# Optimization experiments

Measured on AMD Instinct MI355X. Metric: run time of the kernel, lower is better.

## Reference

```python
import jax, jax.numpy as jnp
import numpy as np

# Dims: batch B, seq L, embed D, router hidden H, num_blocks NB, top_k K
B, L, D, H, NB, K = 8, 4096, 1024, 64, 16, 2
TEMP = 2.0          # current_temperature buffer (init 2.0), clamp(min=0.1) inert
LN_EPS = 1e-5


def setup_inputs() -> dict:
    key = jax.random.key(0)
    k_x, k_w1, k_w2 = jax.random.split(key, 3)
    return {
        "x": jax.random.normal(k_x, (B, L, D), dtype=jnp.float32),
        "ln_gamma": jnp.ones((D,), dtype=jnp.float32),
        "ln_beta": jnp.zeros((D,), dtype=jnp.float32),
        "W1": jax.random.normal(k_w1, (D, H), dtype=jnp.float32) / np.sqrt(D).astype(np.float32),
        "W2": jax.random.normal(k_w2, (H, NB), dtype=jnp.float32) / np.sqrt(H).astype(np.float32),
    }


def reference(x, ln_gamma, ln_beta, W1, W2):
    # gate: LayerNorm -> Linear(no bias) -> GELU(exact) -> Linear(no bias)
    mu = jnp.mean(x, axis=-1, keepdims=True)
    var = jnp.mean(jnp.square(x - mu), axis=-1, keepdims=True)
    xn = (x - mu) * jax.lax.rsqrt(var + LN_EPS) * ln_gamma + ln_beta
    h = jax.nn.gelu(xn @ W1, approximate=False)          # (B, L, H)
    logits = (h @ W2) / TEMP                              # (B, L, NB)

    probs = jax.nn.softmax(logits, axis=-1)               # (B, L, NB)
    top_probs, indices = jax.lax.top_k(probs, K)          # (B, L, K) each
    weights = top_probs / (jnp.sum(top_probs, axis=-1, keepdims=True) + 1e-8)

    # load-balancing aux loss: f = fraction of assignments per block (detached),
    # P = mean router prob per block
    counts = jnp.zeros((NB,), dtype=probs.dtype).at[indices.reshape(-1)].add(1.0)
    f = jax.lax.stop_gradient(counts) / (B * L * K + 1e-8)
    P = jnp.mean(probs, axis=(0, 1))                      # (NB,)
    aux_loss = NB * jnp.sum(f * P)

    return probs, indices, aux_loss, weights
```

## Files before the change

### kernel.cpp

```cpp
#include <hip/hip_runtime.h>
#include <math.h>

typedef __attribute__((ext_vector_type(8))) short short8;
typedef __attribute__((ext_vector_type(4))) float f32x4;

#define NTOK 32768
#define DDIM 1024
#define HDIM 64
#define NB 16
#define LN_EPS 1e-5f

#define IDX_OFF ((size_t)NTOK * NB)
#define AUX_OFF (IDX_OFF + (size_t)NTOK * 2)
#define WT_OFF  (AUX_OFF + 1)

#define CS_F   64
#define BP_F   4352
#define PART_F 102656

__device__ __forceinline__ short8 as_s8(uint4 u) {
    union { uint4 u; short8 s; } x; x.u = u; return x.s;
}

__device__ __forceinline__ f32x4 ntload4(const float* p) {
    return __builtin_nontemporal_load((const f32x4*)p);
}

__device__ __forceinline__ void gld16(const void* g, float* l) {
    __builtin_amdgcn_global_load_lds(
        (const __attribute__((address_space(1))) void*)g,
        (__attribute__((address_space(3))) void*)l, 16, 0, 0);
}

__global__ void pack_kernel(const float* __restrict__ W1,
                            const float* __restrict__ gamma,
                            const float* __restrict__ beta,
                            float* __restrict__ ws) {
    __shared__ float sg[4][64];
    __shared__ float sb[4][64];
    const int s = blockIdx.x;
    const int t = threadIdx.x;

    {
        const int j = t & 63, p = t >> 6;
        float ag = 0.f, ab = 0.f;
        for (int kk = 0; kk < 8; ++kk) {
            const int k = s * 32 + p * 8 + kk;
            const float w = W1[k * HDIM + j];
            ag += gamma[k] * w;
            ab += beta[k] * w;
        }
        sg[p][j] = ag;
        sb[p][j] = ab;
    }

    {
        unsigned int* bp = (unsigned int*)(ws + BP_F);
        const int n = t >> 6;
        const int l = t & 63;
        const int q = l >> 4, c = l & 15;
        const int col = n * 16 + c;
        unsigned int uh[8], um[8], ul[8];
#pragma unroll
        for (int j = 0; j < 8; ++j) {
            const int k = s * 32 + q * 8 + j;
            const float w = gamma[k] * W1[k * HDIM + col];
            const unsigned int hb = __float_as_uint(w) & 0xFFFF0000u;
            const float r = w - __uint_as_float(hb);
            const unsigned int mb = __float_as_uint(r) & 0xFFFF0000u;
            const float r2 = r - __uint_as_float(mb);
            const unsigned int lb = __float_as_uint(r2) & 0xFFFF0000u;
            uh[j] = hb >> 16; um[j] = mb >> 16; ul[j] = lb >> 16;
        }
        const int base = ((s * 4 + n) * 64 + l) * 4;
#pragma unroll
        for (int d = 0; d < 4; ++d) {
            bp[base + d]         = uh[2 * d] | (uh[2 * d + 1] << 16);
            bp[32768 + base + d] = um[2 * d] | (um[2 * d + 1] << 16);
            bp[65536 + base + d] = ul[2 * d] | (ul[2 * d + 1] << 16);
        }
    }
    __syncthreads();
    if (t < 64) {
        atomicAdd(&ws[CS_F + t],      sg[0][t] + sg[1][t] + sg[2][t] + sg[3][t]);
        atomicAdd(&ws[CS_F + 64 + t], sb[0][t] + sb[1][t] + sb[2][t] + sb[3][t]);
    }
}

__device__ __forceinline__ void split8(const f32x4 a0, const f32x4 a1,
                                       short8& AH, short8& AM, short8& AL,
                                       float& s1, float& s2) {
    const float v[8] = {a0.x, a0.y, a0.z, a0.w, a1.x, a1.y, a1.z, a1.w};
    unsigned int ph[4], pm[4], pl[4];
#pragma unroll
    for (int d = 0; d < 4; ++d) {
        const float v0 = v[2 * d], v1 = v[2 * d + 1];
        const unsigned int h0 = __float_as_uint(v0) & 0xFFFF0000u;
        const unsigned int h1 = __float_as_uint(v1) & 0xFFFF0000u;
        const float r0 = v0 - __uint_as_float(h0);
        const float r1 = v1 - __uint_as_float(h1);
        const unsigned int m0 = __float_as_uint(r0) & 0xFFFF0000u;
        const unsigned int m1 = __float_as_uint(r1) & 0xFFFF0000u;
        const float q0 = r0 - __uint_as_float(m0);
        const float q1 = r1 - __uint_as_float(m1);
        ph[d] = (h0 >> 16) | h1;
        pm[d] = (m0 >> 16) | m1;
        pl[d] = (__float_as_uint(q0) >> 16) | (__float_as_uint(q1) & 0xFFFF0000u);
        s1 += v0 + v1;
        s2 = fmaf(v0, v0, fmaf(v1, v1, s2));
    }
    AH = as_s8(make_uint4(ph[0], ph[1], ph[2], ph[3]));
    AM = as_s8(make_uint4(pm[0], pm[1], pm[2], pm[3]));
    AL = as_s8(make_uint4(pl[0], pl[1], pl[2], pl[3]));
}

#define MFMA6(ACC, AH, AM, AL, BH, BM, BL)                                        \
    ACC = __builtin_amdgcn_mfma_f32_16x16x32_bf16(AH, as_s8(BH), ACC, 0, 0, 0);   \
    ACC = __builtin_amdgcn_mfma_f32_16x16x32_bf16(AH, as_s8(BM), ACC, 0, 0, 0);   \
    ACC = __builtin_amdgcn_mfma_f32_16x16x32_bf16(AM, as_s8(BH), ACC, 0, 0, 0);   \
    ACC = __builtin_amdgcn_mfma_f32_16x16x32_bf16(AH, as_s8(BL), ACC, 0, 0, 0);   \
    ACC = __builtin_amdgcn_mfma_f32_16x16x32_bf16(AM, as_s8(BM), ACC, 0, 0, 0);   \
    ACC = __builtin_amdgcn_mfma_f32_16x16x32_bf16(AL, as_s8(BH), ACC, 0, 0, 0);

#define PUB()                                                       \
    asm volatile("s_waitcnt vmcnt(0) lgkmcnt(0)" ::: "memory");     \
    __builtin_amdgcn_s_barrier();                                   \
    __builtin_amdgcn_sched_barrier(0)

#define A_F 0
#define A_BSTRIDE 8704
#define B_F 17408
#define B_BSTRIDE 6144
__global__ __launch_bounds__(512, 2)
void router_main(const float* __restrict__ x,
                 const float* __restrict__ ws_ro,
                 const unsigned int* __restrict__ bp,
                 const float* __restrict__ W2,
                 float* __restrict__ part,
                 float* __restrict__ out) {
    __shared__ __align__(16) float smem[29696];
    float* hlds = smem;
    float* w2l  = smem + 8320;
    float* llds = smem + 9344;
    float* cntl = smem + 11904;

    const int t    = threadIdx.x;
    const int wv   = t >> 6;
    const int lane = t & 63;
    const int q = lane >> 4, c = lane & 15;
    const int tok0 = blockIdx.x * 128;
    const int tokw = tok0 + wv * 16;

    float csg[4], csb[4];
#pragma unroll
    for (int n = 0; n < 4; ++n) {
        csg[n] = ws_ro[CS_F + n * 16 + c];
        csb[n] = ws_ro[CS_F + 64 + n * 16 + c];
    }

    const int bidx0 = wv * 3;
    const float* xA = x + (size_t)(tokw + q) * DDIM + c * 4;
    float* awb       = smem + A_F + wv * 1088 + q * 68 + c * 4;
    const float* arb = smem + A_F + wv * 1088 + c * 68 + q * 8;

#define STAGE_B(CI)                                                              \
    {                                                                            \
        float* dst = smem + B_F + ((CI) & 1) * B_BSTRIDE;                        \
        _Pragma("unroll")                                                        \
        for (int i = 0; i < 3; ++i) {                                            \
            const int idx = bidx0 + i;                                           \
            const int st = (idx >= 12) ? 1 : 0;                                  \
            const int rem = idx - st * 12;                                       \
            const int term = rem >> 2, n = rem & 3;                              \
            gld16(bp + term * 32768 + (2 * (CI) + st) * 1024 + n * 256 + lane*4, \
                  dst + st * 3072 + term * 1024 + n * 256);                      \
        }                                                                        \
    }
#define STAGE_A(CI)                                                              \
    {                                                                            \
        const float* srcA = xA + (CI) * 64;                                      \
        ar0 = ntload4(srcA);                                                     \
        ar1 = ntload4(srcA + 4096);                                              \
        ar2 = ntload4(srcA + 8192);                                              \
        ar3 = ntload4(srcA + 12288);                                             \
    }
#define DS_WRITE_A(CI)                                                           \
    {                                                                            \
        float* dw = awb + ((CI) & 1) * A_BSTRIDE;                                \
        *(f32x4*)(dw)       = ar0;                                               \
        *(f32x4*)(dw + 272) = ar1;                                               \
        *(f32x4*)(dw + 544) = ar2;                                               \
        *(f32x4*)(dw + 816) = ar3;                                               \
    }
#define COMPUTE(CI)                                                              \
    {                                                                            \
        const float* Ab = arb + ((CI) & 1) * A_BSTRIDE;                          \
        const float* Bb = smem + B_F + ((CI) & 1) * B_BSTRIDE;                   \
        _Pragma("unroll")                                                        \
        for (int st = 0; st < 2; ++st) {                                         \
            const f32x4 a00 = *(const f32x4*)(Ab + st * 32);                     \
            const f32x4 a01 = *(const f32x4*)(Ab + st * 32 + 4);                 \
            short8 AH0, AM0, AL0;                                                \
            split8(a00, a01, AH0, AM0, AL0, s1a, s2a);                           \
            const float* Bs = Bb + st * 3072;                                    \
            _Pragma("unroll")                                                    \
            for (int n = 0; n < 4; ++n) {                                        \
                const uint4 bh = *(const uint4*)(Bs + n * 256 + lane * 4);       \
                const uint4 bm = *(const uint4*)(Bs + 1024 + n * 256 + lane*4);  \
                const uint4 bl = *(const uint4*)(Bs + 2048 + n * 256 + lane*4);  \
                MFMA6(acc[n], AH0, AM0, AL0, bh, bm, bl);                        \
            }                                                                    \
        }                                                                        \
    }

    f32x4 acc[4] = {{0.f,0.f,0.f,0.f},{0.f,0.f,0.f,0.f},{0.f,0.f,0.f,0.f},{0.f,0.f,0.f,0.f}};
    float s1a = 0.f, s2a = 0.f;
    f32x4 ar0, ar1, ar2, ar3;

    STAGE_A(0)
    STAGE_B(0)
    DS_WRITE_A(0)
    PUB();

#pragma unroll 1
    for (int ci = 0; ci < 16; ++ci) {
        if (ci < 15) {
            STAGE_A(ci + 1)
            STAGE_B(ci + 1)
            __builtin_amdgcn_sched_barrier(0);
        }
        COMPUTE(ci)
        if (ci < 15) {
            DS_WRITE_A(ci + 1)
            PUB();
        }
    }
    __syncthreads();

    s1a += __shfl_xor(s1a, 16, 64); s1a += __shfl_xor(s1a, 32, 64);
    s2a += __shfl_xor(s2a, 16, 64); s2a += __shfl_xor(s2a, 32, 64);

    if (t < 16) cntl[t] = 0.f;
    if (t < 256) *(float4*)(w2l + t * 4) = *(const float4*)(W2 + t * 4);

    {
        float* hw = hlds + wv * 1040;
#pragma unroll
        for (int r = 0; r < 4; ++r) {
            const int tt = q * 4 + r;
            const float S1A = __shfl(s1a, tt, 64), S2A = __shfl(s2a, tt, 64);
            const float muA = S1A * (1.0f / 1024.0f);
            const float rsA = 1.0f / sqrtf(S2A * (1.0f / 1024.0f) - muA * muA + LN_EPS);
#pragma unroll
            for (int n = 0; n < 4; ++n) {
                const float preA = rsA * (acc[n][r] - muA * csg[n]) + csb[n];
                hw[tt * 65 + n * 16 + c] =
                    0.5f * preA * (1.0f + erff(preA * 0.70710678118654752f));
            }
        }
    }
    __syncthreads();

    {
        const int m2 = t >> 2, o = (t & 3) * 4;
        const float* hrow = hlds + (m2 >> 4) * 1040 + (m2 & 15) * 65;
        f32x4 L0 = {0.f, 0.f, 0.f, 0.f};
#pragma unroll 8
        for (int j = 0; j < 64; ++j) {
            L0 += *(const f32x4*)(w2l + j * 16 + o) * hrow[j];
        }
        *(f32x4*)(llds + m2 * 20 + o) = L0 * 0.5f;
    }
    __syncthreads();

    if (t < 128) {
        float p[16];
        float mx = -1e30f;
#pragma unroll
        for (int i = 0; i < NB; ++i) { p[i] = llds[t * 20 + i]; mx = fmaxf(mx, p[i]); }
        float ssum = 0.f;
#pragma unroll
        for (int i = 0; i < NB; ++i) { p[i] = expf(p[i] - mx); ssum += p[i]; }
        const float inv = 1.0f / ssum;
#pragma unroll
        for (int i = 0; i < NB; ++i) { p[i] *= inv; llds[t * 20 + i] = p[i]; }

        float* po = out + (size_t)(tok0 + t) * NB;
#pragma unroll
        for (int u = 0; u < 4; ++u) {
            float4 v; v.x = p[u*4]; v.y = p[u*4+1]; v.z = p[u*4+2]; v.w = p[u*4+3];
            *(float4*)(po + u * 4) = v;
        }

        float b0 = -1.f, b1 = -1.f;
        int i0 = 0, i1 = 0;
#pragma unroll
        for (int i = 0; i < NB; ++i) {
            if (p[i] > b0)      { b1 = b0; i1 = i0; b0 = p[i]; i0 = i; }
            else if (p[i] > b1) { b1 = p[i]; i1 = i; }
        }
        const float wsum = b0 + b1 + 1e-8f;
        out[IDX_OFF + (size_t)(tok0 + t) * 2]     = (float)i0;
        out[IDX_OFF + (size_t)(tok0 + t) * 2 + 1] = (float)i1;
        out[WT_OFF + (size_t)(tok0 + t) * 2]      = b0 / wsum;
        out[WT_OFF + (size_t)(tok0 + t) * 2 + 1]  = b1 / wsum;
        atomicAdd(&cntl[i0], 1.0f);
        atomicAdd(&cntl[i1], 1.0f);
    }
    __syncthreads();

    if (t < 16) {
        float ps = 0.f;
        for (int m = 0; m < 128; ++m) ps += llds[m * 20 + t];
        part[(size_t)blockIdx.x * 32 + t]      = cntl[t];
        part[(size_t)blockIdx.x * 32 + 16 + t] = ps;
    }
}

__global__ void aux_kernel(const float* __restrict__ part,
                           float* __restrict__ gacc,
                           float* __restrict__ out) {
    __shared__ float red[8][32];
    __shared__ float flag;
    const int t = threadIdx.x;
    const int b = blockIdx.x;
    const int i = t & 31, rr = t >> 5;
    const int r0 = b * 16 + rr;
    red[rr][i] = part[(size_t)r0 * 32 + i] + part[(size_t)(r0 + 8) * 32 + i];
    __syncthreads();
    if (t < 32) {
        float tot = 0.f;
#pragma unroll
        for (int p = 0; p < 8; ++p) tot += red[p][t];
        atomicAdd(&gacc[t], tot);
    }
    __syncthreads();
    if (t == 0) {
        __threadfence();
        const unsigned int old = atomicAdd((unsigned int*)(gacc + 32), 1u);
        flag = (old == 15u) ? 1.f : 0.f;
    }
    __syncthreads();
    if (flag != 0.f) {
        if (t < 32) red[0][t] = atomicAdd(&gacc[t], 0.0f);
        __syncthreads();
        if (t == 0) {
            float a = 0.f;
            for (int k = 0; k < NB; ++k) {
                const float f = red[0][k] / (65536.0f + 1e-8f);
                const float P = red[0][16 + k] * (1.0f / 32768.0f);
                a += f * P;
            }
            out[AUX_OFF] = 16.0f * a;
        }
    }
}

extern "C" void kernel_launch(void* const* d_in, const int* in_sizes, int n_in,
                              void* d_out, int out_size, void* d_ws, size_t ws_size,
                              hipStream_t stream) {
    const float* x     = (const float*)d_in[0];
    const float* gamma = (const float*)d_in[1];
    const float* beta  = (const float*)d_in[2];
    const float* W1    = (const float*)d_in[3];
    const float* W2    = (const float*)d_in[4];
    float* out = (float*)d_out;
    float* ws  = (float*)d_ws;

    (void)hipMemsetAsync(ws, 0, 192 * sizeof(float), stream);
    pack_kernel<<<32, 256, 0, stream>>>(W1, gamma, beta, ws);
    router_main<<<NTOK / 128, 512, 0, stream>>>(x, ws, (const unsigned int*)(ws + BP_F),
                                                W2, ws + PART_F, out);
    aux_kernel<<<16, 256, 0, stream>>>(ws + PART_F, ws, out);
}
```

Baseline: 222.6 us.

## Halve router block size, single-buffer A in LDS, recompute LN column sums per block

Router blocks shrink from 512 threads and 128 tokens to 256 threads and 64 tokens, with a smaller shared-memory footprint. The A tile is now single-buffered with padded stride 65, and x is read with plain loads instead of nontemporal ones. The gamma/beta column sums move out of pack_kernel: each block recomputes them from W1 into LDS, which adds redundant reads of W1. Per-block aux partials are atomically added straight into global accumulators, so the aux kernel becomes one small block; this trades a two-stage reduction for more atomic contention.

```diff
diff --git a/kernel.cpp b/kernel.cpp
--- a/kernel.cpp
+++ b/kernel.cpp
@@ -14,16 +14,10 @@
 #define AUX_OFF (IDX_OFF + (size_t)NTOK * 2)
 #define WT_OFF  (AUX_OFF + 1)
 
-#define CS_F   64
 #define BP_F   4352
-#define PART_F 102656
 
 __device__ __forceinline__ short8 as_s8(uint4 u) {
     union { uint4 u; short8 s; } x; x.u = u; return x.s;
-}
-
-__device__ __forceinline__ f32x4 ntload4(const float* p) {
-    return __builtin_nontemporal_load((const f32x4*)p);
 }
 
 __device__ __forceinline__ void gld16(const void* g, float* l) {
@@ -34,56 +28,32 @@
 
 __global__ void pack_kernel(const float* __restrict__ W1,
                             const float* __restrict__ gamma,
-                            const float* __restrict__ beta,
                             float* __restrict__ ws) {
-    __shared__ float sg[4][64];
-    __shared__ float sb[4][64];
     const int s = blockIdx.x;
     const int t = threadIdx.x;
-
-    {
-        const int j = t & 63, p = t >> 6;
-        float ag = 0.f, ab = 0.f;
-        for (int kk = 0; kk < 8; ++kk) {
-            const int k = s * 32 + p * 8 + kk;
-            const float w = W1[k * HDIM + j];
-            ag += gamma[k] * w;
-            ab += beta[k] * w;
-        }
-        sg[p][j] = ag;
-        sb[p][j] = ab;
-    }
-
-    {
-        unsigned int* bp = (unsigned int*)(ws + BP_F);
-        const int n = t >> 6;
-        const int l = t & 63;
-        const int q = l >> 4, c = l & 15;
-        const int col = n * 16 + c;
-        unsigned int uh[8], um[8], ul[8];
-#pragma unroll
-        for (int j = 0; j < 8; ++j) {
-            const int k = s * 32 + q * 8 + j;
-            const float w = gamma[k] * W1[k * HDIM + col];
-            const unsigned int hb = __float_as_uint(w) & 0xFFFF0000u;
-            const float r = w - __uint_as_float(hb);
-            const unsigned int mb = __float_as_uint(r) & 0xFFFF0000u;
-            const float r2 = r - __uint_as_float(mb);
-            const unsigned int lb = __float_as_uint(r2) & 0xFFFF0000u;
-            uh[j] = hb >> 16; um[j] = mb >> 16; ul[j] = lb >> 16;
-        }
-        const int base = ((s * 4 + n) * 64 + l) * 4;
-#pragma unroll
-        for (int d = 0; d < 4; ++d) {
-            bp[base + d]         = uh[2 * d] | (uh[2 * d + 1] << 16);
-            bp[32768 + base + d] = um[2 * d] | (um[2 * d + 1] << 16);
-            bp[65536 + base + d] = ul[2 * d] | (ul[2 * d + 1] << 16);
-        }
-    }
-    __syncthreads();
-    if (t < 64) {
-        atomicAdd(&ws[CS_F + t],      sg[0][t] + sg[1][t] + sg[2][t] + sg[3][t]);
-        atomicAdd(&ws[CS_F + 64 + t], sb[0][t] + sb[1][t] + sb[2][t] + sb[3][t]);
+    unsigned int* bp = (unsigned int*)(ws + BP_F);
+    const int n = t >> 6;
+    const int l = t & 63;
+    const int q = l >> 4, c = l & 15;
+    const int col = n * 16 + c;
+    unsigned int uh[8], um[8], ul[8];
+#pragma unroll
+    for (int j = 0; j < 8; ++j) {
+        const int k = s * 32 + q * 8 + j;
+        const float w = gamma[k] * W1[k * HDIM + col];
+        const unsigned int hb = __float_as_uint(w) & 0xFFFF0000u;
+        const float r = w - __uint_as_float(hb);
+        const unsigned int mb = __float_as_uint(r) & 0xFFFF0000u;
+        const float r2 = r - __uint_as_float(mb);
+        const unsigned int lb = __float_as_uint(r2) & 0xFFFF0000u;
+        uh[j] = hb >> 16; um[j] = mb >> 16; ul[j] = lb >> 16;
+    }
+    const int base = ((s * 4 + n) * 64 + l) * 4;
+#pragma unroll
+    for (int d = 0; d < 4; ++d) {
+        bp[base + d]         = uh[2 * d] | (uh[2 * d + 1] << 16);
+        bp[32768 + base + d] = um[2 * d] | (um[2 * d + 1] << 16);
+        bp[65536 + base + d] = ul[2 * d] | (ul[2 * d + 1] << 16);
     }
 }
 
@@ -127,47 +97,63 @@
     __builtin_amdgcn_s_barrier();                                   \
     __builtin_amdgcn_sched_barrier(0)
 
-#define A_F 0
-#define A_BSTRIDE 8704
-#define B_F 17408
-#define B_BSTRIDE 6144
-__global__ __launch_bounds__(512, 2)
+__global__ __launch_bounds__(256, 2)
 void router_main(const float* __restrict__ x,
-                 const float* __restrict__ ws_ro,
+                 const float* __restrict__ W1,
+                 const float* __restrict__ gamma,
+                 const float* __restrict__ beta,
                  const unsigned int* __restrict__ bp,
                  const float* __restrict__ W2,
-                 float* __restrict__ part,
+                 float* __restrict__ gacc,
                  float* __restrict__ out) {
-    __shared__ __align__(16) float smem[29696];
-    float* hlds = smem;
-    float* w2l  = smem + 8320;
-    float* llds = smem + 9344;
-    float* cntl = smem + 11904;
+    __shared__ __align__(16) float smem[16592];
+    float* csgl = smem + 16448;
+    float* csbl = smem + 16512;
+    float* cntl = smem + 16576;
+    float* w2l  = smem;
+    float* llds = smem + 1024;
+    float* hlds = smem + 12288;
 
     const int t    = threadIdx.x;
     const int wv   = t >> 6;
     const int lane = t & 63;
     const int q = lane >> 4, c = lane & 15;
-    const int tok0 = blockIdx.x * 128;
+    const int tok0 = blockIdx.x * 64;
     const int tokw = tok0 + wv * 16;
 
-    float csg[4], csb[4];
-#pragma unroll
-    for (int n = 0; n < 4; ++n) {
-        csg[n] = ws_ro[CS_F + n * 16 + c];
-        csb[n] = ws_ro[CS_F + 64 + n * 16 + c];
-    }
-
-    const int bidx0 = wv * 3;
+    {
+        const int j = t & 63, p = t >> 6;
+        float ag = 0.f, ab = 0.f;
+#pragma unroll 4
+        for (int k = p; k < DDIM; k += 4) {
+            const float w = W1[k * HDIM + j];
+            ag = fmaf(gamma[k], w, ag);
+            ab = fmaf(beta[k],  w, ab);
+        }
+        float* red = smem + 12288;
+        red[p * 64 + j] = ag;
+        red[256 + p * 64 + j] = ab;
+        __syncthreads();
+        if (t < 64)
+            csgl[t] = red[t] + red[64 + t] + red[128 + t] + red[192 + t];
+        else if (t < 128) {
+            const int j2 = t - 64;
+            csbl[j2] = red[256 + j2] + red[320 + j2] + red[384 + j2] + red[448 + j2];
+        }
+        if (t < 16) cntl[t] = 0.f;
+        __syncthreads();
+    }
+
+    const int bidx0 = wv * 6;
     const float* xA = x + (size_t)(tokw + q) * DDIM + c * 4;
-    float* awb       = smem + A_F + wv * 1088 + q * 68 + c * 4;
-    const float* arb = smem + A_F + wv * 1088 + c * 68 + q * 8;
+    float* awb       = smem + 12288 + wv * 1040 + q * 65 + c * 4;
+    const float* arb = smem + 12288 + wv * 1040 + c * 65 + q * 8;
 
 #define STAGE_B(CI)                                                              \
     {                                                                            \
-        float* dst = smem + B_F + ((CI) & 1) * B_BSTRIDE;                        \
+        float* dst = smem + ((CI) & 1) * 6144;                                   \
         _Pragma("unroll")                                                        \
-        for (int i = 0; i < 3; ++i) {                                            \
+        for (int i = 0; i < 6; ++i) {                                            \
             const int idx = bidx0 + i;                                           \
             const int st = (idx >= 12) ? 1 : 0;                                  \
             const int rem = idx - st * 12;                                       \
@@ -179,27 +165,25 @@
 #define STAGE_A(CI)                                                              \
     {                                                                            \
         const float* srcA = xA + (CI) * 64;                                      \
-        ar0 = ntload4(srcA);                                                     \
-        ar1 = ntload4(srcA + 4096);                                              \
-        ar2 = ntload4(srcA + 8192);                                              \
-        ar3 = ntload4(srcA + 12288);                                             \
-    }
-#define DS_WRITE_A(CI)                                                           \
+        ar0 = *(const f32x4*)(srcA);                                             \
+        ar1 = *(const f32x4*)(srcA + 4096);                                      \
+        ar2 = *(const f32x4*)(srcA + 8192);                                      \
+        ar3 = *(const f32x4*)(srcA + 12288);                                     \
+    }
+#define DS_WRITE_A()                                                             \
     {                                                                            \
-        float* dw = awb + ((CI) & 1) * A_BSTRIDE;                                \
-        *(f32x4*)(dw)       = ar0;                                               \
-        *(f32x4*)(dw + 272) = ar1;                                               \
-        *(f32x4*)(dw + 544) = ar2;                                               \
-        *(f32x4*)(dw + 816) = ar3;                                               \
+        *(f32x4*)(awb)       = ar0;                                              \
+        *(f32x4*)(awb + 260) = ar1;                                              \
+        *(f32x4*)(awb + 520) = ar2;                                              \
+        *(f32x4*)(awb + 780) = ar3;                                              \
     }
 #define COMPUTE(CI)                                                              \
     {                                                                            \
-        const float* Ab = arb + ((CI) & 1) * A_BSTRIDE;                          \
-        const float* Bb = smem + B_F + ((CI) & 1) * B_BSTRIDE;                   \
+        const float* Bb = smem + ((CI) & 1) * 6144;                              \
         _Pragma("unroll")                                                        \
         for (int st = 0; st < 2; ++st) {                                         \
-            const f32x4 a00 = *(const f32x4*)(Ab + st * 32);                     \
-            const f32x4 a01 = *(const f32x4*)(Ab + st * 32 + 4);                 \
+            const f32x4 a00 = *(const f32x4*)(arb + st * 32);                    \
+            const f32x4 a01 = *(const f32x4*)(arb + st * 32 + 4);                \
             short8 AH0, AM0, AL0;                                                \
             split8(a00, a01, AH0, AM0, AL0, s1a, s2a);                           \
             const float* Bs = Bb + st * 3072;                                    \
@@ -219,7 +203,7 @@
 
     STAGE_A(0)
     STAGE_B(0)
-    DS_WRITE_A(0)
+    DS_WRITE_A()
     PUB();
 
 #pragma unroll 1
@@ -230,8 +214,10 @@
             __builtin_amdgcn_sched_barrier(0);
         }
         COMPUTE(ci)
+        asm volatile("s_waitcnt lgkmcnt(0)" ::: "memory");
+        __builtin_amdgcn_sched_barrier(0);
         if (ci < 15) {
-            DS_WRITE_A(ci + 1)
+            DS_WRITE_A()
             PUB();
         }
     }
@@ -240,8 +226,7 @@
     s1a += __shfl_xor(s1a, 16, 64); s1a += __shfl_xor(s1a, 32, 64);
     s2a += __shfl_xor(s2a, 16, 64); s2a += __shfl_xor(s2a, 32, 64);
 
-    if (t < 16) cntl[t] = 0.f;
-    if (t < 256) *(float4*)(w2l + t * 4) = *(const float4*)(W2 + t * 4);
+    *(float4*)(w2l + t * 4) = *(const float4*)(W2 + t * 4);
 
     {
         float* hw = hlds + wv * 1040;
@@ -253,7 +238,8 @@
             const float rsA = 1.0f / sqrtf(S2A * (1.0f / 1024.0f) - muA * muA + LN_EPS);
 #pragma unroll
             for (int n = 0; n < 4; ++n) {
-                const float preA = rsA * (acc[n][r] - muA * csg[n]) + csb[n];
+                const float preA = rsA * (acc[n][r] - muA * csgl[n * 16 + c])
+                                 + csbl[n * 16 + c];
                 hw[tt * 65 + n * 16 + c] =
                     0.5f * preA * (1.0f + erff(preA * 0.70710678118654752f));
             }
@@ -273,7 +259,7 @@
     }
     __syncthreads();
 
-    if (t < 128) {
+    if (t < 64) {
         float p[16];
         float mx = -1e30f;
 #pragma unroll
@@ -311,48 +297,26 @@
 
     if (t < 16) {
         float ps = 0.f;
-        for (int m = 0; m < 128; ++m) ps += llds[m * 20 + t];
-        part[(size_t)blockIdx.x * 32 + t]      = cntl[t];
-        part[(size_t)blockIdx.x * 32 + 16 + t] = ps;
-    }
-}
-
-__global__ void aux_kernel(const float* __restrict__ part,
-                           float* __restrict__ gacc,
+        for (int m = 0; m < 64; ++m) ps += llds[m * 20 + t];
+        atomicAdd(&gacc[t], cntl[t]);
+        atomicAdd(&gacc[16 + t], ps);
+    }
+}
+
+__global__ void aux_kernel(float* __restrict__ gacc,
                            float* __restrict__ out) {
-    __shared__ float red[8][32];
-    __shared__ float flag;
+    __shared__ float red[32];
     const int t = threadIdx.x;
-    const int b = blockIdx.x;
-    const int i = t & 31, rr = t >> 5;
-    const int r0 = b * 16 + rr;
-    red[rr][i] = part[(size_t)r0 * 32 + i] + part[(size_t)(r0 + 8) * 32 + i];
-    __syncthreads();
-    if (t < 32) {
-        float tot = 0.f;
-#pragma unroll
-        for (int p = 0; p < 8; ++p) tot += red[p][t];
-        atomicAdd(&gacc[t], tot);
-    }
+    if (t < 32) red[t] = atomicAdd(&gacc[t], 0.0f);
     __syncthreads();
     if (t == 0) {
-        __threadfence();
-        const unsigned int old = atomicAdd((unsigned int*)(gacc + 32), 1u);
-        flag = (old == 15u) ? 1.f : 0.f;
-    }
-    __syncthreads();
-    if (flag != 0.f) {
-        if (t < 32) red[0][t] = atomicAdd(&gacc[t], 0.0f);
-        __syncthreads();
-        if (t == 0) {
-            float a = 0.f;
-            for (int k = 0; k < NB; ++k) {
-                const float f = red[0][k] / (65536.0f + 1e-8f);
-                const float P = red[0][16 + k] * (1.0f / 32768.0f);
-                a += f * P;
-            }
-            out[AUX_OFF] = 16.0f * a;
-        }
+        float a = 0.f;
+        for (int k = 0; k < NB; ++k) {
+            const float f = red[k] / (65536.0f + 1e-8f);
+            const float P = red[16 + k] * (1.0f / 32768.0f);
+            a += f * P;
+        }
+        out[AUX_OFF] = 16.0f * a;
     }
 }
 
@@ -368,8 +332,9 @@
     float* ws  = (float*)d_ws;
 
     (void)hipMemsetAsync(ws, 0, 192 * sizeof(float), stream);
-    pack_kernel<<<32, 256, 0, stream>>>(W1, gamma, beta, ws);
-    router_main<<<NTOK / 128, 512, 0, stream>>>(x, ws, (const unsigned int*)(ws + BP_F),
-                                                W2, ws + PART_F, out);
-    aux_kernel<<<16, 256, 0, stream>>>(ws + PART_F, ws, out);
-}
+    pack_kernel<<<32, 256, 0, stream>>>(W1, gamma, ws);
+    router_main<<<NTOK / 64, 256, 0, stream>>>(x, W1, gamma, beta,
+                                               (const unsigned int*)(ws + BP_F),
+                                               W2, ws, out);
+    aux_kernel<<<1, 64, 0, stream>>>(ws, out);
+}
```

Result: slower. 238.4 us (+7.1%).
